# Optimization experiments

Measured on AMD Instinct MI355X. Metric: run time of the kernel, lower is better.

## Reference

```python
import jax, jax.numpy as jnp
import numpy as np

B, S, D = 4, 2048, 1024
LN_EPS = 1e-5
NEG_INF = -1e9


def _layernorm(x, gamma, beta):
    mu = jnp.mean(x, axis=-1, keepdims=True)
    var = jnp.var(x, axis=-1, keepdims=True)
    return (x - mu) * jax.lax.rsqrt(var + LN_EPS) * gamma + beta


def setup_inputs() -> dict:
    key = jax.random.key(0)
    k1, k2, k3, k4 = jax.random.split(key, 4)
    context = jax.random.normal(k1, (B, S, D), dtype=jnp.float32)
    eos_mask = jnp.ones((B, S, S), dtype=jnp.int64)
    prior = jax.random.uniform(k2, (B, S, S), dtype=jnp.float32)
    bound = 1.0 / np.sqrt(D)
    Wq = jax.random.uniform(k3, (D, D), dtype=jnp.float32, minval=-bound, maxval=bound)
    Wk = jax.random.uniform(k4, (D, D), dtype=jnp.float32, minval=-bound, maxval=bound)
    gamma = jnp.ones((D,), dtype=jnp.float32)
    beta = jnp.zeros((D,), dtype=jnp.float32)
    return {"context": context, "eos_mask": eos_mask, "prior": prior,
            "Wq": Wq, "Wk": Wk, "gamma": gamma, "beta": beta}


def reference(context, eos_mask, prior, Wq, Wk, gamma, beta):
    d_model = context.shape[-1]
    seq_len = context.shape[1]
    x = _layernorm(context, gamma, beta)
    q = x @ Wq.T                                   # nn.Linear, no bias
    k = x @ Wk.T
    scores = jnp.einsum('bsd,btd->bst', q, k) / jnp.sqrt(jnp.asarray(d_model, x.dtype))

    idx = jnp.arange(seq_len)
    a_sup = idx[:, None] + 1 == idx[None, :]       # superdiagonal (torch `a`)
    c_sub = idx[:, None] - 1 == idx[None, :]       # subdiagonal  (torch `c`)
    diag = idx[:, None] == idx[None, :]            # identity     (torch `b`)
    strict_lower = idx[:, None] > idx[None, :]     # tril - eye

    # mask = eos_mask & (a + c)  (Python precedence: & binds looser than +)
    mask = (eos_mask != 0) & (a_sup | c_sub)
    scores = jnp.where(mask, scores, NEG_INF)
    neibor_attn = jax.nn.softmax(scores, axis=-1)
    neibor_attn = jnp.sqrt(neibor_attn * jnp.swapaxes(neibor_attn, -1, -2) + 1e-9)
    neibor_attn = prior + (1.0 - prior) * neibor_attn

    # t = log(neibor+1e-9).masked_fill(a==0,0) @ tril  == reverse cumsum over last axis
    logn = jnp.where(a_sup, jnp.log(neibor_attn + 1e-9), 0.0)
    t = jnp.cumsum(logn[:, :, ::-1], axis=-1)[:, :, ::-1]
    # g = exp(tril @ t), keep strictly-lower part ((tril - eye) != 0)
    g = jnp.exp(jnp.cumsum(t, axis=1))
    g = jnp.where(strict_lower, g, 0.0)

    g_attn = g + jnp.swapaxes(g, -1, -2) + jnp.where(diag, neibor_attn, 1e-9)
    return g_attn, neibor_attn
```

## Files before the change

### kernel.cpp

```cpp
#include <hip/hip_runtime.h>
#include <hip/hip_bf16.h>
#include <stdint.h>

#define SS 2048
#define DD 1024
#define RR 8192

typedef _Float16 f16;
typedef _Float16 f16x8 __attribute__((ext_vector_type(8)));
typedef _Float16 f16x4 __attribute__((ext_vector_type(4)));
typedef float    f32x4 __attribute__((ext_vector_type(4)));

__device__ __forceinline__ void gl_lds16(const f16* g, f16* l) {
  __builtin_amdgcn_global_load_lds((const __attribute__((address_space(1))) void*)g,
                                   (__attribute__((address_space(3))) void*)l,
                                   16, 0, 0);
}

__global__ __launch_bounds__(256) void k_pre(const float* __restrict__ x,
                                             const float* __restrict__ gamma,
                                             const float* __restrict__ beta,
                                             f16* __restrict__ xn,
                                             const float* __restrict__ Wq,
                                             const float* __restrict__ Wk,
                                             f16* __restrict__ Wqt,
                                             f16* __restrict__ Wkt) {
  __shared__ f16 tile[64][72];
  int bidx = blockIdx.x;
  int t = threadIdx.x;
  if (bidx < RR) {
    int lane = t & 63, w = t >> 6;
    const float* xr = x + (size_t)bidx * DD;
    float4 v = ((const float4*)xr)[t];
    float s  = v.x + v.y + v.z + v.w;
    float ss = v.x*v.x + v.y*v.y + v.z*v.z + v.w*v.w;
#pragma unroll
    for (int off = 32; off > 0; off >>= 1) {
      s  += __shfl_down(s,  off, 64);
      ss += __shfl_down(ss, off, 64);
    }
    float* r0 = (float*)&tile[0][0];
    float* r1 = r0 + 4;
    if (lane == 0) { r0[w] = s; r1[w] = ss; }
    __syncthreads();
    float tot = r0[0]+r0[1]+r0[2]+r0[3];
    float tss = r1[0]+r1[1]+r1[2]+r1[3];
    float mu  = tot * (1.0f/DD);
    float var = tss * (1.0f/DD) - mu*mu;
    float inv = rsqrtf(var + 1e-5f);
    float4 g = ((const float4*)gamma)[t];
    float4 b = ((const float4*)beta)[t];
    f16x4 o;
    o[0] = (f16)((v.x-mu)*inv*g.x + b.x);
    o[1] = (f16)((v.y-mu)*inv*g.y + b.y);
    o[2] = (f16)((v.z-mu)*inv*g.z + b.z);
    o[3] = (f16)((v.w-mu)*inv*g.w + b.w);
    *(f16x4*)(xn + (size_t)bidx*DD + t*4) = o;
  } else {
    int bid = bidx - RR;
    const float* src = (bid & 1) ? Wk : Wq;
    f16* dst = (bid & 1) ? Wkt : Wqt;
    int tb = bid >> 1;
    int r0 = (tb >> 4) << 6, c0 = (tb & 15) << 6;
#pragma unroll
    for (int p = 0; p < 4; ++p) {
      int r = p * 16 + (t >> 4);
      int c = (t & 15) * 4;
      float4 v = *(const float4*)(src + (size_t)(r0 + r) * DD + c0 + c);
      tile[c + 0][r] = (f16)v.x; tile[c + 1][r] = (f16)v.y;
      tile[c + 2][r] = (f16)v.z; tile[c + 3][r] = (f16)v.w;
    }
    __syncthreads();
    int orow = t >> 2, och = (t & 3) * 16;
    f16x8 a = *(const f16x8*)&tile[orow][och];
    f16x8 b = *(const f16x8*)&tile[orow][och + 8];
    f16* o = dst + (size_t)(c0 + orow) * DD + r0 + och;
    *(f16x8*)o = a;
    *(f16x8*)(o + 8) = b;
  }
}

template<int BM, int BN, int LOG2NBN>
__global__ __launch_bounds__(256) void k_gemm_t(const f16* __restrict__ A,
                                                const f16* __restrict__ Bw,
                                                f16* __restrict__ C) {
  constexpr int K  = 1024;
  constexpr int NC = 1024;
  constexpr int MF = BM / 32;
  constexpr int NF = BN / 32;
  constexpr int IA = BM / 64;
  constexpr int IB = BN / 64;
  __shared__ f16 As[BM * 32];
  __shared__ f16 Bs[BN * 32];
  int cpx = gridDim.x >> 3;
  int bid = (blockIdx.x & 7) * cpx + (blockIdx.x >> 3);
  int bm = bid >> LOG2NBN, bn = bid & ((1 << LOG2NBN) - 1);
  int tid = threadIdx.x;
  int lane = tid & 63, w = tid >> 6;
  int wm = w >> 1, wn = w & 1;

  f32x4 acc[MF][NF] = {};

  int srow = w * 16 + (lane >> 2);
  int sch  = lane & 3;
  const f16* AgI[IA];
  const f16* BgI[IB];
  f16* lAI[IA];
  f16* lBI[IB];
#pragma unroll
  for (int i = 0; i < IA; ++i) {
    AgI[i] = A + (size_t)(bm * BM + i * 64 + srow) * K + sch * 8;
    lAI[i] = As + (i * 64 + w * 16) * 32;
  }
#pragma unroll
  for (int i = 0; i < IB; ++i) {
    BgI[i] = Bw + (size_t)(bn * BN + i * 64 + srow) * K + sch * 8;
    lBI[i] = Bs + (i * 64 + w * 16) * 32;
  }

  int rlo = lane & 15, rch = (lane >> 4) * 8;

  for (int kt = 0; kt < K; kt += 32) {
    __syncthreads();
#pragma unroll
    for (int i = 0; i < IA; ++i) gl_lds16(AgI[i] + kt, lAI[i]);
#pragma unroll
    for (int i = 0; i < IB; ++i) gl_lds16(BgI[i] + kt, lBI[i]);
    __syncthreads();
    f16x8 af[MF], bf[NF];
#pragma unroll
    for (int mi = 0; mi < MF; ++mi)
      af[mi] = *(const f16x8*)(As + (wm * (BM/2) + mi * 16 + rlo) * 32 + rch);
#pragma unroll
    for (int ni = 0; ni < NF; ++ni)
      bf[ni] = *(const f16x8*)(Bs + (wn * (BN/2) + ni * 16 + rlo) * 32 + rch);
#pragma unroll
    for (int mi = 0; mi < MF; ++mi)
#pragma unroll
      for (int ni = 0; ni < NF; ++ni)
        acc[mi][ni] = __builtin_amdgcn_mfma_f32_16x16x32_f16(af[mi], bf[ni], acc[mi][ni], 0, 0, 0);
  }
  int c0 = (lane >> 4) * 4;
#pragma unroll
  for (int mi = 0; mi < MF; ++mi)
#pragma unroll
    for (int ni = 0; ni < NF; ++ni)
#pragma unroll
      for (int r = 0; r < 4; ++r) {
        int row = bm * BM + wm * (BM/2) + mi * 16 + c0 + r;
        int col = bn * BN + wn * (BN/2) + ni * 16 + rlo;
        C[(size_t)row * NC + col] = (f16)acc[mi][ni][r];
      }
}

__global__ __launch_bounds__(256) void k_dots(const f16* __restrict__ Xn,
                                              const f16* __restrict__ Y,
                                              const int* __restrict__ eos,
                                              const float* __restrict__ prior,
                                              float* __restrict__ sup,
                                              float* __restrict__ sub,
                                              int* __restrict__ e_sup,
                                              int* __restrict__ e_sub,
                                              float* __restrict__ pr_sup) {
  int q = (int)gridDim.x >> 3, r7 = (int)gridDim.x & 7;
  int xcd = blockIdx.x & 7, idx = blockIdx.x >> 3;
  int sb = (xcd < r7 ? xcd * (q + 1) : r7 * (q + 1) + (xcd - r7) * q) + idx;
  int pair = sb * 4 + (threadIdx.x >> 6);
  int lane = threadIdx.x & 63;
  int b = pair / 2047;
  int s = pair - b * 2047;
  size_t r0 = ((size_t)(b * SS + s)) * DD;
  size_t r1 = r0 + DD;
  int d0 = lane * 16;
  float da = 0.f, dc = 0.f;
#pragma unroll
  for (int h = 0; h < 2; ++h) {
    f16x8 xs  = *(const f16x8*)(Xn + r0 + d0 + h*8);
    f16x8 ys1 = *(const f16x8*)(Y  + r1 + d0 + h*8);
    f16x8 ys  = *(const f16x8*)(Y  + r0 + d0 + h*8);
    f16x8 xs1 = *(const f16x8*)(Xn + r1 + d0 + h*8);
#pragma unroll
    for (int e = 0; e < 8; ++e) {
      da += (float)xs[e] * (float)ys1[e];
      dc += (float)ys[e] * (float)xs1[e];
    }
  }
#pragma unroll
  for (int off = 32; off > 0; off >>= 1) {
    da += __shfl_down(da, off, 64);
    dc += __shfl_down(dc, off, 64);
  }
  size_t ebase = (size_t)b * SS * SS;
  int bS = b * SS;
  if (lane == 0) {
    sup[bS + s]     = da * 0.03125f;
    sub[bS + s + 1] = dc * 0.03125f;
  } else if (lane == 1) {
    e_sup[bS + s] = eos[ebase + (size_t)s * SS + s + 1];
  } else if (lane == 2) {
    e_sub[bS + s + 1] = eos[ebase + (size_t)(s + 1) * SS + s];
  } else if (lane == 3) {
    pr_sup[bS + s] = prior[ebase + (size_t)s * SS + s + 1];
  }
}

__global__ __launch_bounds__(1024) void k_scan(const float* __restrict__ sup,
                                               const float* __restrict__ sub,
                                               const int* __restrict__ e_sup,
                                               const int* __restrict__ e_sub,
                                               const float* __restrict__ pr_sup,
                                               float* __restrict__ p_sup,
                                               float* __restrict__ p_sub,
                                               double* __restrict__ P) {
  int b = blockIdx.x, t = threadIdx.x;
  int lane = t & 63, wid = t >> 6;
  int bS = b * SS;
  __shared__ float  psub_sh[SS];
  __shared__ double wsum[16];
  float psup_loc[2];
#pragma unroll
  for (int e = 0; e < 2; ++e) {
    int s = 2*t + e;
    bool supOK = (s < SS-1) && (e_sup[bS + s] != 0);
    bool subOK = (s >= 1)   && (e_sub[bS + s] != 0);
    float ps = 0.f, pb = 0.f;
    if (supOK && subOK) {
      float Av = sup[bS + s], Cv = sub[bS + s];
      float m  = fmaxf(Av, Cv);
      float ea = expf(Av - m), eb = expf(Cv - m);
      float iv = 1.0f / (ea + eb);
      ps = ea * iv; pb = eb * iv;
    } else if (supOK) ps = 1.f;
    else if (subOK)   pb = 1.f;
    p_sup[bS + s] = ps; p_sub[bS + s] = pb;
    psub_sh[s] = pb; psup_loc[e] = ps;
  }
  __syncthreads();
  double L0 = 0.0, L1 = 0.0;
#pragma unroll
  for (int e = 0; e < 2; ++e) {
    int s = 2*t + e;
    double Lv = 0.0;
    if (s < SS-1) {
      float pr = pr_sup[bS + s];
      float vv = sqrtf(psup_loc[e] * psub_sh[s+1] + 1e-9f);
      Lv = (double)logf(pr + (1.f - pr)*vv + 1e-9f);
    }
    if (e == 0) L0 = Lv; else L1 = Lv;
  }
  double pairv = L0 + L1;
  double v = pairv;
#pragma unroll
  for (int off = 1; off < 64; off <<= 1) {
    double u = __shfl_up(v, off, 64);
    if (lane >= off) v += u;
  }
  if (lane == 63) wsum[wid] = v;
  __syncthreads();
  double base = 0.0;
  for (int wI = 0; wI < wid; ++wI) base += wsum[wI];
  double excl = base + v - pairv;
  P[bS + 2*t]     = excl + L0;
  P[bS + 2*t + 1] = excl + L0 + L1;
}

__global__ __launch_bounds__(256) void k_out(const float* __restrict__ prior,
                                             const float* __restrict__ p_sup,
                                             const float* __restrict__ p_sub,
                                             const double* __restrict__ P,
                                             float* __restrict__ g_out,
                                             float* __restrict__ n_out) {
  size_t v = (size_t)blockIdx.x * 256 + threadIdx.x;
  int j4   = (int)(v & 511);
  int rowg = (int)(v >> 9);
  int s = rowg & (SS - 1);
  int b = rowg >> 11;
  size_t base = (size_t)rowg * SS + j4 * 4;
  union F4 { float4 v4; float a[4]; };
  F4 prf; prf.v4 = *(const float4*)(prior + base);
  int bS = b * SS;
  double Ps  = P[bS + s];
  double Ps2 = (s >= 2) ? P[bS + s - 2] : 0.0;
  const float SQ9 = 3.1622776601683795e-5f;
  F4 gv, nv;
#pragma unroll
  for (int e = 0; e < 4; ++e) {
    int j = j4*4 + e;
    float pr = prf.a[e];
    float vv;
    if (j == s + 1)      vv = sqrtf(p_sup[bS+s] * p_sub[bS+s+1] + 1e-9f);
    else if (j == s - 1) vv = sqrtf(p_sub[bS+s] * p_sup[bS+s-1] + 1e-9f);
    else                 vv = SQ9;
    float na = pr + (1.f - pr) * vv;
    nv.a[e] = na;
    float g;
    if (s == j) g = na;
    else if (s > j) {
      double Pj2 = (j >= 2) ? P[bS + j - 2] : 0.0;
      g = expf((float)(Ps - Pj2)) + 1e-9f;
    } else {
      g = expf((float)(P[bS + j] - Ps2)) + 1e-9f;
    }
    gv.a[e] = g;
  }
  *(float4*)(g_out + base) = gv.v4;
  *(float4*)(n_out + base) = nv.v4;
}

extern "C" void kernel_launch(void* const* d_in, const int* in_sizes, int n_in,
                              void* d_out, int out_size, void* d_ws, size_t ws_size,
                              hipStream_t stream) {
  const float* context = (const float*)d_in[0];
  const int*   eos     = (const int*)d_in[1];
  const float* prior   = (const float*)d_in[2];
  const float* Wq      = (const float*)d_in[3];
  const float* Wk      = (const float*)d_in[4];
  const float* gamma   = (const float*)d_in[5];
  const float* beta    = (const float*)d_in[6];

  char* ws = (char*)d_ws;
  float*  sup    = (float*)(ws);
  float*  sub    = (float*)(ws + 32768);
  float*  p_sup  = (float*)(ws + 65536);
  float*  p_sub  = (float*)(ws + 98304);
  double* P      = (double*)(ws + 131072);
  int*    e_sup  = (int*)(ws + 196608);
  int*    e_sub  = (int*)(ws + 229376);
  float*  pr_sup = (float*)(ws + 262144);
  const size_t smallEnd = 294912;

  const size_t XN_BYTES = (size_t)RR * DD * 2;
  const size_t Y_BYTES  = (size_t)RR * DD * 2;
  const size_t WT_BYTES = (size_t)DD * DD * 2;
  const size_t bigNeed  = XN_BYTES + Y_BYTES + 3 * WT_BYTES;
  char* big;
  if (ws_size >= smallEnd + bigNeed) big = ws + smallEnd;
  else big = (char*)d_out + ((size_t)out_size * 4 - bigNeed);
  f16* Xn  = (f16*)big;
  f16* Y   = (f16*)(big + XN_BYTES);
  f16* Wqt = (f16*)(big + XN_BYTES + Y_BYTES);
  f16* Wkt = (f16*)(big + XN_BYTES + Y_BYTES + WT_BYTES);
  f16* Mm  = (f16*)(big + XN_BYTES + Y_BYTES + 2 * WT_BYTES);

  k_pre<<<RR + 512, 256, 0, stream>>>(context, gamma, beta, Xn, Wq, Wk, Wqt, Wkt);
  k_gemm_t<64, 64, 4><<<256, 256, 0, stream>>>(Wqt, Wkt, Mm);
  k_gemm_t<128, 128, 3><<<512, 256, 0, stream>>>(Xn, Mm, Y);
  k_dots<<<2047, 256, 0, stream>>>(Xn, Y, eos, prior, sup, sub, e_sup, e_sub, pr_sup);
  k_scan<<<4, 1024, 0, stream>>>(sup, sub, e_sup, e_sub, pr_sup, p_sup, p_sub, P);
  float* g_out = (float*)d_out;
  float* n_out = g_out + (size_t)RR * SS;
  k_out<<<16384, 256, 0, stream>>>(prior, p_sup, p_sub, P, g_out, n_out);
}
```

Baseline: 120.4 us.

## Fuse neighbor dot products into big GEMM epilogue, drop Y buffer and k_dots

The Xn·M GEMM epilogue now loads a slab of Xn rows (plus one halo row on each side) into LDS and computes the superdiagonal and subdiagonal dot products directly from the accumulators. Partial sums across column tiles are combined with atomicAdd into sup/sub. The eos/prior gathers and the zeroing of sup/sub move into extra blocks of k_pre. This removes the write and re-read of the 16 MB Y intermediate and one kernel launch, at the cost of extra LDS use, shuffles and float atomics, which also make the sums non-deterministic in order.

```diff
diff --git a/kernel.cpp b/kernel.cpp
--- a/kernel.cpp
+++ b/kernel.cpp
@@ -24,7 +24,14 @@
                                              const float* __restrict__ Wq,
                                              const float* __restrict__ Wk,
                                              f16* __restrict__ Wqt,
-                                             f16* __restrict__ Wkt) {
+                                             f16* __restrict__ Wkt,
+                                             const int* __restrict__ eos,
+                                             const float* __restrict__ prior,
+                                             float* __restrict__ sup_g,
+                                             float* __restrict__ sub_g,
+                                             int* __restrict__ e_sup,
+                                             int* __restrict__ e_sub,
+                                             float* __restrict__ pr_sup) {
   __shared__ f16 tile[64][72];
   int bidx = blockIdx.x;
   int t = threadIdx.x;
@@ -56,7 +63,7 @@
     o[2] = (f16)((v.z-mu)*inv*g.z + b.z);
     o[3] = (f16)((v.w-mu)*inv*g.w + b.w);
     *(f16x4*)(xn + (size_t)bidx*DD + t*4) = o;
-  } else {
+  } else if (bidx < RR + 512) {
     int bid = bidx - RR;
     const float* src = (bid & 1) ? Wk : Wq;
     f16* dst = (bid & 1) ? Wkt : Wqt;
@@ -77,21 +84,39 @@
     f16* o = dst + (size_t)(c0 + orow) * DD + r0 + och;
     *(f16x8*)o = a;
     *(f16x8*)(o + 8) = b;
-  }
-}
-
-template<int BM, int BN, int LOG2NBN>
+  } else {
+    int g = bidx - (RR + 512);
+    int u = g * 256 + t;
+    sup_g[u] = 0.f;
+    sub_g[u] = 0.f;
+    if (u < 4 * 2047) {
+      int b = u / 2047;
+      int s = u - b * 2047;
+      size_t ebase = (size_t)b * SS * SS;
+      int bS = b * SS;
+      e_sup[bS + s]     = eos[ebase + (size_t)s * SS + s + 1];
+      e_sub[bS + s + 1] = eos[ebase + (size_t)(s + 1) * SS + s];
+      pr_sup[bS + s]    = prior[ebase + (size_t)s * SS + s + 1];
+    }
+  }
+}
+
+template<int BM, int BN, int LOG2NBN, bool FUSE>
 __global__ __launch_bounds__(256) void k_gemm_t(const f16* __restrict__ A,
                                                 const f16* __restrict__ Bw,
-                                                f16* __restrict__ C) {
+                                                f16* __restrict__ C,
+                                                float* __restrict__ sup_g,
+                                                float* __restrict__ sub_g) {
   constexpr int K  = 1024;
   constexpr int NC = 1024;
   constexpr int MF = BM / 32;
   constexpr int NF = BN / 32;
   constexpr int IA = BM / 64;
   constexpr int IB = BN / 64;
+  constexpr int XST = 136;
   __shared__ f16 As[BM * 32];
   __shared__ f16 Bs[BN * 32];
+  __shared__ f16 Xs[FUSE ? 130 * XST : 1];
   int cpx = gridDim.x >> 3;
   int bid = (blockIdx.x & 7) * cpx + (blockIdx.x >> 3);
   int bm = bid >> LOG2NBN, bn = bid & ((1 << LOG2NBN) - 1);
@@ -141,66 +166,58 @@
         acc[mi][ni] = __builtin_amdgcn_mfma_f32_16x16x32_f16(af[mi], bf[ni], acc[mi][ni], 0, 0, 0);
   }
   int c0 = (lane >> 4) * 4;
-#pragma unroll
-  for (int mi = 0; mi < MF; ++mi)
-#pragma unroll
-    for (int ni = 0; ni < NF; ++ni)
+  if constexpr (!FUSE) {
+#pragma unroll
+    for (int mi = 0; mi < MF; ++mi)
+#pragma unroll
+      for (int ni = 0; ni < NF; ++ni)
+#pragma unroll
+        for (int r = 0; r < 4; ++r) {
+          int row = bm * BM + wm * (BM/2) + mi * 16 + c0 + r;
+          int col = bn * BN + wn * (BN/2) + ni * 16 + rlo;
+          C[(size_t)row * NC + col] = (f16)acc[mi][ni][r];
+        }
+  } else {
+    int slabBase = bm * BM - 1;
+#pragma unroll
+    for (int it = 0; it < 9; ++it) {
+      int c = tid + it * 256;
+      if (c < 130 * 16) {
+        int rI = c >> 4, colc = (c & 15) * 8;
+        int gr = slabBase + rI;
+        gr = gr < 0 ? 0 : (gr > RR - 1 ? RR - 1 : gr);
+        *(f16x8*)(Xs + rI * XST + colc) =
+            *(const f16x8*)(A + (size_t)gr * K + bn * BN + colc);
+      }
+    }
+    __syncthreads();
+#pragma unroll
+    for (int mi = 0; mi < MF; ++mi) {
 #pragma unroll
       for (int r = 0; r < 4; ++r) {
-        int row = bm * BM + wm * (BM/2) + mi * 16 + c0 + r;
-        int col = bn * BN + wn * (BN/2) + ni * 16 + rlo;
-        C[(size_t)row * NC + col] = (f16)acc[mi][ni][r];
+        int rloc = wm * (BM/2) + mi * 16 + c0 + r;
+        float su = 0.f, sb = 0.f;
+#pragma unroll
+        for (int ni = 0; ni < NF; ++ni) {
+          float y = acc[mi][ni][r];
+          int colL = wn * (BN/2) + ni * 16 + rlo;
+          su += y * (float)Xs[rloc * XST + colL];
+          sb += y * (float)Xs[(rloc + 2) * XST + colL];
+        }
+#pragma unroll
+        for (int m = 1; m < 16; m <<= 1) {
+          su += __shfl_xor(su, m, 64);
+          sb += __shfl_xor(sb, m, 64);
+        }
+        if (rlo == 0) {
+          int rho = bm * BM + rloc;
+          if ((rho & (SS - 1)) != 0)
+            atomicAdd(&sup_g[rho - 1], su * 0.03125f);
+          if ((rho & (SS - 1)) != SS - 1)
+            atomicAdd(&sub_g[rho + 1], sb * 0.03125f);
+        }
       }
-}
-
-__global__ __launch_bounds__(256) void k_dots(const f16* __restrict__ Xn,
-                                              const f16* __restrict__ Y,
-                                              const int* __restrict__ eos,
-                                              const float* __restrict__ prior,
-                                              float* __restrict__ sup,
-                                              float* __restrict__ sub,
-                                              int* __restrict__ e_sup,
-                                              int* __restrict__ e_sub,
-                                              float* __restrict__ pr_sup) {
-  int q = (int)gridDim.x >> 3, r7 = (int)gridDim.x & 7;
-  int xcd = blockIdx.x & 7, idx = blockIdx.x >> 3;
-  int sb = (xcd < r7 ? xcd * (q + 1) : r7 * (q + 1) + (xcd - r7) * q) + idx;
-  int pair = sb * 4 + (threadIdx.x >> 6);
-  int lane = threadIdx.x & 63;
-  int b = pair / 2047;
-  int s = pair - b * 2047;
-  size_t r0 = ((size_t)(b * SS + s)) * DD;
-  size_t r1 = r0 + DD;
-  int d0 = lane * 16;
-  float da = 0.f, dc = 0.f;
-#pragma unroll
-  for (int h = 0; h < 2; ++h) {
-    f16x8 xs  = *(const f16x8*)(Xn + r0 + d0 + h*8);
-    f16x8 ys1 = *(const f16x8*)(Y  + r1 + d0 + h*8);
-    f16x8 ys  = *(const f16x8*)(Y  + r0 + d0 + h*8);
-    f16x8 xs1 = *(const f16x8*)(Xn + r1 + d0 + h*8);
-#pragma unroll
-    for (int e = 0; e < 8; ++e) {
-      da += (float)xs[e] * (float)ys1[e];
-      dc += (float)ys[e] * (float)xs1[e];
-    }
-  }
-#pragma unroll
-  for (int off = 32; off > 0; off >>= 1) {
-    da += __shfl_down(da, off, 64);
-    dc += __shfl_down(dc, off, 64);
-  }
-  size_t ebase = (size_t)b * SS * SS;
-  int bS = b * SS;
-  if (lane == 0) {
-    sup[bS + s]     = da * 0.03125f;
-    sub[bS + s + 1] = dc * 0.03125f;
-  } else if (lane == 1) {
-    e_sup[bS + s] = eos[ebase + (size_t)s * SS + s + 1];
-  } else if (lane == 2) {
-    e_sub[bS + s + 1] = eos[ebase + (size_t)(s + 1) * SS + s];
-  } else if (lane == 3) {
-    pr_sup[bS + s] = prior[ebase + (size_t)s * SS + s + 1];
+    }
   }
 }
 
@@ -330,22 +347,20 @@
   const size_t smallEnd = 294912;
 
   const size_t XN_BYTES = (size_t)RR * DD * 2;
-  const size_t Y_BYTES  = (size_t)RR * DD * 2;
   const size_t WT_BYTES = (size_t)DD * DD * 2;
-  const size_t bigNeed  = XN_BYTES + Y_BYTES + 3 * WT_BYTES;
+  const size_t bigNeed  = XN_BYTES + 3 * WT_BYTES;
   char* big;
   if (ws_size >= smallEnd + bigNeed) big = ws + smallEnd;
   else big = (char*)d_out + ((size_t)out_size * 4 - bigNeed);
   f16* Xn  = (f16*)big;
-  f16* Y   = (f16*)(big + XN_BYTES);
-  f16* Wqt = (f16*)(big + XN_BYTES + Y_BYTES);
-  f16* Wkt = (f16*)(big + XN_BYTES + Y_BYTES + WT_BYTES);
-  f16* Mm  = (f16*)(big + XN_BYTES + Y_BYTES + 2 * WT_BYTES);
-
-  k_pre<<<RR + 512, 256, 0, stream>>>(context, gamma, beta, Xn, Wq, Wk, Wqt, Wkt);
-  k_gemm_t<64, 64, 4><<<256, 256, 0, stream>>>(Wqt, Wkt, Mm);
-  k_gemm_t<128, 128, 3><<<512, 256, 0, stream>>>(Xn, Mm, Y);
-  k_dots<<<2047, 256, 0, stream>>>(Xn, Y, eos, prior, sup, sub, e_sup, e_sub, pr_sup);
+  f16* Wqt = (f16*)(big + XN_BYTES);
+  f16* Wkt = (f16*)(big + XN_BYTES + WT_BYTES);
+  f16* Mm  = (f16*)(big + XN_BYTES + 2 * WT_BYTES);
+
+  k_pre<<<RR + 512 + 32, 256, 0, stream>>>(context, gamma, beta, Xn, Wq, Wk, Wqt, Wkt,
+                                           eos, prior, sup, sub, e_sup, e_sub, pr_sup);
+  k_gemm_t<64, 64, 4, false><<<256, 256, 0, stream>>>(Wqt, Wkt, Mm, nullptr, nullptr);
+  k_gemm_t<128, 128, 3, true><<<512, 256, 0, stream>>>(Xn, Mm, nullptr, sup, sub);
   k_scan<<<4, 1024, 0, stream>>>(sup, sub, e_sup, e_sub, pr_sup, p_sup, p_sub, P);
   float* g_out = (float*)d_out;
   float* n_out = g_out + (size_t)RR * SS;
```

Measured after the change: 105.1 us (median of 3 runs). 12.7% less time.
